# Kernel optimization log

Measured on AMD Instinct MI355X. Metric: run time of the kernel, lower is better.

The kernel has to match this reference:

```python
import math
import jax, jax.numpy as jnp
import numpy as np

# ---- module hyperparameters (from init_kwargs) ----
BIG_K = 13
SMALL_K = 3
C_OUT = 128
GROUP_IN = 4
NK = math.ceil(BIG_K / SMALL_K)          # 5 small kernels cover the big one
C_IN = NK * C_OUT                        # 640
PADDING = SMALL_K - 1                    # shift() padding
EXTRA_PAD = PADDING - SMALL_K // 2       # 1
MID = BIG_K // 2
REAL_PAD = [MID - i * SMALL_K - PADDING for i in range(NK)]  # [4,1,-2,-5,-8]
MARGIN = BIG_K                           # zero-pad margin covering all shifts

B = 32
HOUT = 56
WOUT = 56
HIN = HOUT + 2 * EXTRA_PAD
WIN = WOUT + 2 * EXTRA_PAD


def _build_indices():
    # Faithful numpy replication of shuffle_idx_2_gen_pads (torch.manual_seed(123) analog).
    rng = np.random.RandomState(123)
    idx_offset = np.array(REAL_PAD * C_OUT, dtype=np.int32)  # (C_IN,)

    def group_pads():
        pads = []
        for _ in range(GROUP_IN):
            idx = np.concatenate([rng.permutation(NK) + i * NK for i in range(C_OUT)])
            pads.append(idx_offset[np.argsort(idx, kind='stable')])
        return np.stack(pads)  # (GROUP_IN, C_IN)

    pad_h = group_pads()
    pad_v = group_pads()
    pad_hv = np.concatenate([pad_h, pad_v], axis=0).T.astype(np.int32)  # (C_IN, 2*GROUP_IN)
    idx_identit = np.stack(
        [rng.randint(0, NK, C_OUT) + np.arange(C_OUT) * NK for _ in range(GROUP_IN)]
    ).T.astype(np.int32)  # (C_OUT, GROUP_IN)
    return pad_hv, idx_identit


def setup_inputs() -> dict:
    key = jax.random.key(0)
    pad_hv, idx_identit = _build_indices()
    x = jax.random.normal(key, (B, C_IN, HIN, WIN), dtype=jnp.float32)
    return {
        'x': x,
        'pad_hv': jnp.asarray(pad_hv),
        'idx_identit': jnp.asarray(idx_identit),
        'hout': HOUT,
        'wout': WOUT,
    }


def reference(x, pad_hv, idx_identit, hout, wout):
    # x: (B, C_IN, hout+2*EXTRA_PAD, wout+2*EXTRA_PAD)
    Bx = x.shape[0]
    M = MARGIN

    # ---- horizontal-shift branch: per-channel shift along W, accumulate over groups ----
    xp_w = jnp.pad(x, ((0, 0), (0, 0), (0, 0), (M, M)))          # zero pad width
    xh = xp_w[:, :, EXTRA_PAD:EXTRA_PAD + hout, :]
    w_base = jnp.arange(wout, dtype=jnp.int32) + EXTRA_PAD + M   # (wout,)
    out_h = jnp.zeros((Bx, C_IN, hout, wout), x.dtype)
    for g in range(GROUP_IN):
        idx = w_base[None, :] + pad_hv[:, g][:, None]            # (C_IN, wout)
        out_h = out_h + jnp.take_along_axis(xh, idx[None, :, None, :], axis=3)

    # ---- vertical-shift branch: per-channel shift along H ----
    xp_h = jnp.pad(x, ((0, 0), (0, 0), (M, M), (0, 0)))
    xv = xp_h[:, :, :, EXTRA_PAD:EXTRA_PAD + wout]               # (B,C_IN,HIN+2M,wout)
    h_base = jnp.arange(hout, dtype=jnp.int32) + EXTRA_PAD + M
    out_v = jnp.zeros((Bx, C_IN, hout, wout), x.dtype)
    for g in range(GROUP_IN):
        idx = h_base[None, :] + pad_hv[:, GROUP_IN + g][:, None]  # (C_IN, hout)
        out_v = out_v + jnp.take_along_axis(xv, idx[None, :, :, None], axis=2)

    # scatter-add input channels j into output channel idx_out[j] = j // NK
    out_h = out_h.reshape(Bx, C_OUT, NK, hout, wout).sum(axis=2)
    out_v = out_v.reshape(Bx, C_OUT, NK, hout, wout).sum(axis=2)

    # ---- identity branch: center crop + channel gather, summed over groups ----
    xc = x[:, :, EXTRA_PAD:EXTRA_PAD + hout, EXTRA_PAD:EXTRA_PAD + wout]
    out_id = xc[:, idx_identit, :, :].sum(axis=2)                # (B,C_OUT,hout,wout)

    return out_h, out_v, out_id
```

## Files before the change

kernel.cpp:

```cpp
#include <hip/hip_runtime.h>

#define BATCH   32
#define C_OUT_N 128
#define NK      5
#define C_IN_N  (NK * C_OUT_N)
#define HIN     58
#define WIN     58
#define HOUT    56
#define WOUT    56
#define NPIX    (HOUT * WOUT)
#define NTILE   (HOUT * (WOUT / 8))
#define OUT_PLANE ((size_t)BATCH * C_OUT_N * NPIX)

#define NTHREADS   512
#define LDS_STRIDE 70
#define LDS_ROWS   (NK * HIN)
#define LDS_HALVES (LDS_ROWS * LDS_STRIDE)
#define CH_STRIDE  (HIN * LDS_STRIDE)
#define NV4        (NK * HIN * WIN / 4)

typedef _Float16 h2 __attribute__((ext_vector_type(2)));

static __device__ __forceinline__ unsigned int h2u(h2 v) {
    unsigned int r; __builtin_memcpy(&r, &v, 4); return r;
}
static __device__ __forceinline__ h2 uh2(unsigned int u) {
    h2 r; __builtin_memcpy(&r, &u, 4); return r;
}
static __device__ __forceinline__ h2 algn(h2 lo, h2 hi) {
    return uh2(__builtin_amdgcn_alignbit(h2u(hi), h2u(lo), 16));
}
static __device__ __forceinline__ h2 pkrtz(float a, float b) {
    auto t = __builtin_amdgcn_cvt_pkrtz(a, b);
    h2 r; __builtin_memcpy(&r, &t, 4); return r;
}
static __device__ __forceinline__ float uni(float v) {
    return __uint_as_float(__builtin_amdgcn_readfirstlane(__float_as_uint(v)));
}

__global__ __launch_bounds__(NTHREADS, 8) void addshift_hoist_kernel(
    const float* __restrict__ x,
    const int*   __restrict__ pad_hv,
    const int*   __restrict__ idx_id,
    float*       __restrict__ out)
{
    extern __shared__ _Float16 lds[];

    const int bc  = blockIdx.x;
    const int b   = bc / C_OUT_N;
    const int co  = bc - b * C_OUT_N;
    const int tid = threadIdx.x;

    for (int i = tid; i < LDS_ROWS * 12; i += NTHREADS) {
        int j = i / 12;
        int m = i - j * 12;
        int c = (m < 7) ? m : (58 + m);
        lds[j * LDS_STRIDE + c] = (_Float16)0.f;
    }

    const float* xbase = x + (size_t)(b * C_IN_N + co * NK) * (HIN * WIN);
    for (int i = tid; i < NV4; i += NTHREADS) {
        int g = 4 * i;
        float4 v = *(const float4*)(xbase + g);
        int r = g / 58;
        int c = g - r * 58;
        _Float16* dst = &lds[r * LDS_STRIDE + 7 + c];
        if (c <= 54) {
            dst[0] = (_Float16)v.x;
            *(h2*)(dst + 1) = pkrtz(v.y, v.z);
            dst[3] = (_Float16)v.w;
        } else {
            dst[0] = (_Float16)v.x;
            dst[1] = (_Float16)v.y;
            _Float16* d2 = &lds[(r + 1) * LDS_STRIDE + 7];
            d2[0] = (_Float16)v.z;
            d2[1] = (_Float16)v.w;
        }
    }

    float mhf[NK][5], mvf[NK][5], cntf[NK];
    #pragma unroll
    for (int k = 0; k < NK; ++k) {
        #pragma unroll
        for (int t = 0; t < 5; ++t) { mhf[k][t] = 0.f; mvf[k][t] = 0.f; }
        cntf[k] = 0.f;
        #pragma unroll
        for (int g = 0; g < 4; ++g) {
            int sh_v = pad_hv[(co * NK + k) * 8 + g];
            int th   = (4 - sh_v) / 3;
            int sv_v = pad_hv[(co * NK + k) * 8 + 4 + g];
            int tv   = (4 - sv_v) / 3;
            #pragma unroll
            for (int t = 0; t < 5; ++t) {
                mhf[k][t] += (th == t) ? 1.f : 0.f;
                mvf[k][t] += (tv == t) ? 1.f : 0.f;
            }
        }
    }
    #pragma unroll
    for (int g = 0; g < 4; ++g) {
        int c = idx_id[co * 4 + g] - co * NK;
        #pragma unroll
        for (int k = 0; k < NK; ++k) cntf[k] += (c == k) ? 1.f : 0.f;
    }
    #pragma unroll
    for (int k = 0; k < NK; ++k) {
        cntf[k] = uni(cntf[k]);
        #pragma unroll
        for (int t = 0; t < 5; ++t) { mhf[k][t] = uni(mhf[k][t]); mvf[k][t] = uni(mvf[k][t]); }
    }

    __syncthreads();

    const int q = tid;
    if (q < NTILE) {
        const int h  = q / 7;
        const int w0 = 8 * (q - h * 7);

        int  voff[5];
        bool okv[5];
        #pragma unroll
        for (int t = 0; t < 5; ++t) {
            int rr = h + 5 - 3 * t;
            okv[t] = (unsigned)rr < 58u;
            int rc = rr < 0 ? 0 : (rr > 57 ? 57 : rr);
            voff[t] = rc * LDS_STRIDE + w0 + 8;
        }
        const int rowbase = (h + 1) * LDS_STRIDE + w0;

        h2 sh[4], sv[4], si[4];
        #pragma unroll
        for (int m = 0; m < 4; ++m) {
            sh[m] = h2{(_Float16)0.f, (_Float16)0.f};
            sv[m] = sh[m]; si[m] = sh[m];
        }

        #pragma unroll
        for (int k = 0; k < NK; ++k) {
            const _Float16* chp  = lds + k * CH_STRIDE;
            const _Float16* rowp = chp + rowbase;

            h2 H[10];
            #pragma unroll
            for (int m = 0; m < 10; ++m) H[m] = *(const h2*)(rowp + 2 * m);

            h2 V[5][4];
            #pragma unroll
            for (int t = 0; t < 5; ++t) {
                const _Float16* vp = chp + voff[t];
                #pragma unroll
                for (int m = 0; m < 4; ++m) V[t][m] = *(const h2*)(vp + 2 * m);
            }

            #pragma unroll
            for (int t = 0; t < 5; ++t) {
                float wg = mhf[k][t];
                if (wg != 0.f) {
                    _Float16 wh = (_Float16)wg;
                    h2 w2 = h2{wh, wh};
                    int j = 12 - 3 * t;
                    if ((j & 1) == 0) {
                        int m0 = j >> 1;
                        #pragma unroll
                        for (int m = 0; m < 4; ++m) sh[m] += w2 * H[m0 + m];
                    } else {
                        int m0 = (j - 1) >> 1;
                        #pragma unroll
                        for (int m = 0; m < 4; ++m)
                            sh[m] += w2 * algn(H[m0 + m], H[m0 + m + 1]);
                    }
                }
            }

            float ck = cntf[k];
            if (ck != 0.f) {
                _Float16 ch16 = (_Float16)ck;
                h2 c2 = h2{ch16, ch16};
                #pragma unroll
                for (int m = 0; m < 4; ++m) si[m] += c2 * H[4 + m];
            }

            #pragma unroll
            for (int t = 0; t < 5; ++t) {
                float wv = mvf[k][t];
                if (wv != 0.f) {
                    float wm = okv[t] ? wv : 0.f;
                    _Float16 wh = (_Float16)wm;
                    h2 w2 = h2{wh, wh};
                    #pragma unroll
                    for (int m = 0; m < 4; ++m) sv[m] += w2 * V[t][m];
                }
            }
        }

        size_t o = (size_t)bc * NPIX + h * WOUT + w0;
        *(float4*)(out + o) =
            make_float4((float)sh[0].x, (float)sh[0].y, (float)sh[1].x, (float)sh[1].y);
        *(float4*)(out + o + 4) =
            make_float4((float)sh[2].x, (float)sh[2].y, (float)sh[3].x, (float)sh[3].y);
        *(float4*)(out + OUT_PLANE + o) =
            make_float4((float)sv[0].x, (float)sv[0].y, (float)sv[1].x, (float)sv[1].y);
        *(float4*)(out + OUT_PLANE + o + 4) =
            make_float4((float)sv[2].x, (float)sv[2].y, (float)sv[3].x, (float)sv[3].y);
        *(float4*)(out + 2 * OUT_PLANE + o) =
            make_float4((float)si[0].x, (float)si[0].y, (float)si[1].x, (float)si[1].y);
        *(float4*)(out + 2 * OUT_PLANE + o + 4) =
            make_float4((float)si[2].x, (float)si[2].y, (float)si[3].x, (float)si[3].y);
    }
}

extern "C" void kernel_launch(void* const* d_in, const int* in_sizes, int n_in,
                              void* d_out, int out_size, void* d_ws, size_t ws_size,
                              hipStream_t stream) {
    const float* x      = (const float*)d_in[0];
    const int*   pad_hv = (const int*)d_in[1];
    const int*   idx_id = (const int*)d_in[2];
    float*       out    = (float*)d_out;

    addshift_hoist_kernel<<<dim3(BATCH * C_OUT_N), dim3(NTHREADS),
                            LDS_HALVES * 2, stream>>>(x, pad_hv, idx_id, out);
}
```

Baseline: 106.9 us.

## Double-buffer per-channel LDS staging with register prefetch of next channel

Replaces staging all five input channels in LDS at once with a two-slot ring buffer. Each thread prefetches the next channel into registers while the current one is processed. This cuts LDS footprint to raise occupancy and overlaps global loads with compute, at the cost of extra block-wide barriers per channel. Vertical-branch values are now read from LDS on demand instead of preloaded.

```diff
diff --git a/kernel.cpp b/kernel.cpp
--- a/kernel.cpp
+++ b/kernel.cpp
@@ -14,10 +14,9 @@
 
 #define NTHREADS   512
 #define LDS_STRIDE 70
-#define LDS_ROWS   (NK * HIN)
-#define LDS_HALVES (LDS_ROWS * LDS_STRIDE)
-#define CH_STRIDE  (HIN * LDS_STRIDE)
-#define NV4        (NK * HIN * WIN / 4)
+#define CH_HALVES  (HIN * LDS_STRIDE)
+#define LDS_HALVES (2 * CH_HALVES)
+#define NV4C       (HIN * WIN / 4)
 
 typedef _Float16 h2 __attribute__((ext_vector_type(2)));
 
@@ -38,7 +37,7 @@
     return __uint_as_float(__builtin_amdgcn_readfirstlane(__float_as_uint(v)));
 }
 
-__global__ __launch_bounds__(NTHREADS, 8) void addshift_hoist_kernel(
+__global__ __launch_bounds__(NTHREADS, 8) void addshift_pipe_kernel(
     const float* __restrict__ x,
     const int*   __restrict__ pad_hv,
     const int*   __restrict__ idx_id,
@@ -51,20 +50,19 @@
     const int co  = bc - b * C_OUT_N;
     const int tid = threadIdx.x;
 
-    for (int i = tid; i < LDS_ROWS * 12; i += NTHREADS) {
-        int j = i / 12;
-        int m = i - j * 12;
-        int c = (m < 7) ? m : (58 + m);
-        lds[j * LDS_STRIDE + c] = (_Float16)0.f;
-    }
-
     const float* xbase = x + (size_t)(b * C_IN_N + co * NK) * (HIN * WIN);
-    for (int i = tid; i < NV4; i += NTHREADS) {
-        int g = 4 * i;
-        float4 v = *(const float4*)(xbase + g);
+
+    auto issue_ch = [&](int k, float4& v1, float4& v2) {
+        const float* src = xbase + k * (HIN * WIN);
+        v1 = *(const float4*)(src + 4 * tid);
+        if (tid < NV4C - NTHREADS)
+            v2 = *(const float4*)(src + 4 * (tid + NTHREADS));
+    };
+    auto write_one = [&](int bsel, float4 v, int i4) {
+        int g = 4 * i4;
         int r = g / 58;
-        int c = g - r * 58;
-        _Float16* dst = &lds[r * LDS_STRIDE + 7 + c];
+        int c = g - 58 * r;
+        _Float16* dst = &lds[bsel * CH_HALVES + r * LDS_STRIDE + 7 + c];
         if (c <= 54) {
             dst[0] = (_Float16)v.x;
             *(h2*)(dst + 1) = pkrtz(v.y, v.z);
@@ -72,11 +70,27 @@
         } else {
             dst[0] = (_Float16)v.x;
             dst[1] = (_Float16)v.y;
-            _Float16* d2 = &lds[(r + 1) * LDS_STRIDE + 7];
+            _Float16* d2 = &lds[bsel * CH_HALVES + (r + 1) * LDS_STRIDE + 7];
             d2[0] = (_Float16)v.z;
             d2[1] = (_Float16)v.w;
         }
-    }
+    };
+    auto write_ch = [&](int bsel, float4 v1, float4 v2) {
+        write_one(bsel, v1, tid);
+        if (tid < NV4C - NTHREADS) write_one(bsel, v2, tid + NTHREADS);
+    };
+
+    for (int i = tid; i < 2 * HIN * 12; i += NTHREADS) {
+        int bsel = i / (HIN * 12);
+        int m2   = i - bsel * (HIN * 12);
+        int row  = m2 / 12;
+        int m    = m2 - row * 12;
+        int c    = (m < 7) ? m : (58 + m);
+        lds[bsel * CH_HALVES + row * LDS_STRIDE + c] = (_Float16)0.f;
+    }
+
+    float4 s1, s2;
+    issue_ch(0, s1, s2);
 
     float mhf[NK][5], mvf[NK][5], cntf[NK];
     #pragma unroll
@@ -110,47 +124,42 @@
         for (int t = 0; t < 5; ++t) { mhf[k][t] = uni(mhf[k][t]); mvf[k][t] = uni(mvf[k][t]); }
     }
 
+    write_ch(0, s1, s2);
+    issue_ch(1, s1, s2);
     __syncthreads();
 
-    const int q = tid;
-    if (q < NTILE) {
-        const int h  = q / 7;
-        const int w0 = 8 * (q - h * 7);
-
-        int  voff[5];
-        bool okv[5];
-        #pragma unroll
-        for (int t = 0; t < 5; ++t) {
-            int rr = h + 5 - 3 * t;
-            okv[t] = (unsigned)rr < 58u;
-            int rc = rr < 0 ? 0 : (rr > 57 ? 57 : rr);
-            voff[t] = rc * LDS_STRIDE + w0 + 8;
-        }
-        const int rowbase = (h + 1) * LDS_STRIDE + w0;
-
-        h2 sh[4], sv[4], si[4];
-        #pragma unroll
-        for (int m = 0; m < 4; ++m) {
-            sh[m] = h2{(_Float16)0.f, (_Float16)0.f};
-            sv[m] = sh[m]; si[m] = sh[m];
-        }
-
-        #pragma unroll
-        for (int k = 0; k < NK; ++k) {
-            const _Float16* chp  = lds + k * CH_STRIDE;
+    const int q  = tid;
+    const int h  = q / 7;
+    const int w0 = 8 * (q - h * 7);
+    int  voff[5];
+    bool okv[5];
+    #pragma unroll
+    for (int t = 0; t < 5; ++t) {
+        int rr = h + 5 - 3 * t;
+        okv[t] = (unsigned)rr < 58u;
+        int rc = rr < 0 ? 0 : (rr > 57 ? 57 : rr);
+        voff[t] = rc * LDS_STRIDE + w0 + 8;
+    }
+    const int rowbase = (h + 1) * LDS_STRIDE + w0;
+
+    h2 sh[4], sv[4], si[4];
+    #pragma unroll
+    for (int m = 0; m < 4; ++m) {
+        sh[m] = h2{(_Float16)0.f, (_Float16)0.f};
+        sv[m] = sh[m]; si[m] = sh[m];
+    }
+
+    #pragma unroll
+    for (int k = 0; k < NK; ++k) {
+        const int cb = (k & 1) * CH_HALVES;
+
+        if (q < NTILE) {
+            const _Float16* chp  = lds + cb;
             const _Float16* rowp = chp + rowbase;
 
             h2 H[10];
             #pragma unroll
             for (int m = 0; m < 10; ++m) H[m] = *(const h2*)(rowp + 2 * m);
-
-            h2 V[5][4];
-            #pragma unroll
-            for (int t = 0; t < 5; ++t) {
-                const _Float16* vp = chp + voff[t];
-                #pragma unroll
-                for (int m = 0; m < 4; ++m) V[t][m] = *(const h2*)(vp + 2 * m);
-            }
 
             #pragma unroll
             for (int t = 0; t < 5; ++t) {
@@ -174,8 +183,8 @@
 
             float ck = cntf[k];
             if (ck != 0.f) {
-                _Float16 ch16 = (_Float16)ck;
-                h2 c2 = h2{ch16, ch16};
+                _Float16 c16 = (_Float16)ck;
+                h2 c2 = h2{c16, c16};
                 #pragma unroll
                 for (int m = 0; m < 4; ++m) si[m] += c2 * H[4 + m];
             }
@@ -187,12 +196,23 @@
                     float wm = okv[t] ? wv : 0.f;
                     _Float16 wh = (_Float16)wm;
                     h2 w2 = h2{wh, wh};
+                    const _Float16* vp = chp + voff[t];
                     #pragma unroll
-                    for (int m = 0; m < 4; ++m) sv[m] += w2 * V[t][m];
+                    for (int m = 0; m < 4; ++m)
+                        sv[m] += w2 * *(const h2*)(vp + 2 * m);
                 }
             }
         }
 
+        if (k < NK - 1) {
+            __syncthreads();
+            write_ch((k + 1) & 1, s1, s2);
+            if (k < NK - 2) issue_ch(k + 2, s1, s2);
+            __syncthreads();
+        }
+    }
+
+    if (q < NTILE) {
         size_t o = (size_t)bc * NPIX + h * WOUT + w0;
         *(float4*)(out + o) =
             make_float4((float)sh[0].x, (float)sh[0].y, (float)sh[1].x, (float)sh[1].y);
@@ -217,6 +237,6 @@
     const int*   idx_id = (const int*)d_in[2];
     float*       out    = (float*)d_out;
 
-    addshift_hoist_kernel<<<dim3(BATCH * C_OUT_N), dim3(NTHREADS),
-                            LDS_HALVES * 2, stream>>>(x, pad_hv, idx_id, out);
-}
+    addshift_pipe_kernel<<<dim3(BATCH * C_OUT_N), dim3(NTHREADS),
+                           LDS_HALVES * 2, stream>>>(x, pad_hv, idx_id, out);
+}
```

New measurement: 128.6 us. 1.2x slower.

## Make kernel persistent over batches and prefetch next input tile into registers

Applied to the files above, without the earlier changes.

Launches 512 blocks instead of 4096. Each block handles one output channel for eight batch entries, with the pad/identity weight setup done once per block. While the current batch's LDS tile is being computed, the next batch's input is prefetched into registers (eight float4 per thread plus a tail) so the global load overlaps compute. Vertical taps are now loaded on demand instead of all preloaded. This costs register pressure (launch bounds relaxed to 4) and leaves fewer blocks to hide latency and balance load across CUs.

```diff
diff --git a/kernel.cpp b/kernel.cpp
--- a/kernel.cpp
+++ b/kernel.cpp
@@ -18,6 +18,9 @@
 #define LDS_HALVES (LDS_ROWS * LDS_STRIDE)
 #define CH_STRIDE  (HIN * LDS_STRIDE)
 #define NV4        (NK * HIN * WIN / 4)
+#define NFULL      8
+#define NTAIL      (NV4 - NFULL * NTHREADS)
+#define NCHUNK     8
 
 typedef _Float16 h2 __attribute__((ext_vector_type(2)));
 
@@ -38,7 +41,7 @@
     return __uint_as_float(__builtin_amdgcn_readfirstlane(__float_as_uint(v)));
 }
 
-__global__ __launch_bounds__(NTHREADS, 8) void addshift_hoist_kernel(
+__global__ __launch_bounds__(NTHREADS, 4) void addshift_pers_kernel(
     const float* __restrict__ x,
     const int*   __restrict__ pad_hv,
     const int*   __restrict__ idx_id,
@@ -46,9 +49,9 @@
 {
     extern __shared__ _Float16 lds[];
 
-    const int bc  = blockIdx.x;
-    const int b   = bc / C_OUT_N;
-    const int co  = bc - b * C_OUT_N;
+    const int bid = blockIdx.x;
+    const int co  = bid & 127;
+    const int b0  = bid >> 7;
     const int tid = threadIdx.x;
 
     for (int i = tid; i < LDS_ROWS * 12; i += NTHREADS) {
@@ -58,10 +61,8 @@
         lds[j * LDS_STRIDE + c] = (_Float16)0.f;
     }
 
-    const float* xbase = x + (size_t)(b * C_IN_N + co * NK) * (HIN * WIN);
-    for (int i = tid; i < NV4; i += NTHREADS) {
-        int g = 4 * i;
-        float4 v = *(const float4*)(xbase + g);
+    auto write_one = [&](float4 v, int i4) {
+        int g = 4 * i4;
         int r = g / 58;
         int c = g - r * 58;
         _Float16* dst = &lds[r * LDS_STRIDE + 7 + c];
@@ -76,7 +77,7 @@
             d2[0] = (_Float16)v.z;
             d2[1] = (_Float16)v.w;
         }
-    }
+    };
 
     float mhf[NK][5], mvf[NK][5], cntf[NK];
     #pragma unroll
@@ -110,102 +111,124 @@
         for (int t = 0; t < 5; ++t) { mhf[k][t] = uni(mhf[k][t]); mvf[k][t] = uni(mvf[k][t]); }
     }
 
-    __syncthreads();
-
-    const int q = tid;
-    if (q < NTILE) {
-        const int h  = q / 7;
-        const int w0 = 8 * (q - h * 7);
-
-        int  voff[5];
-        bool okv[5];
-        #pragma unroll
-        for (int t = 0; t < 5; ++t) {
-            int rr = h + 5 - 3 * t;
-            okv[t] = (unsigned)rr < 58u;
-            int rc = rr < 0 ? 0 : (rr > 57 ? 57 : rr);
-            voff[t] = rc * LDS_STRIDE + w0 + 8;
-        }
-        const int rowbase = (h + 1) * LDS_STRIDE + w0;
-
-        h2 sh[4], sv[4], si[4];
-        #pragma unroll
-        for (int m = 0; m < 4; ++m) {
-            sh[m] = h2{(_Float16)0.f, (_Float16)0.f};
-            sv[m] = sh[m]; si[m] = sh[m];
-        }
-
-        #pragma unroll
-        for (int k = 0; k < NK; ++k) {
-            const _Float16* chp  = lds + k * CH_STRIDE;
-            const _Float16* rowp = chp + rowbase;
-
-            h2 H[10];
-            #pragma unroll
-            for (int m = 0; m < 10; ++m) H[m] = *(const h2*)(rowp + 2 * m);
-
-            h2 V[5][4];
-            #pragma unroll
-            for (int t = 0; t < 5; ++t) {
-                const _Float16* vp = chp + voff[t];
+    const int h  = tid / 7;
+    const int w0 = 8 * (tid - h * 7);
+    int  voff[5];
+    bool okv[5];
+    #pragma unroll
+    for (int t = 0; t < 5; ++t) {
+        int rr = h + 5 - 3 * t;
+        okv[t] = (unsigned)rr < 58u;
+        int rc = rr < 0 ? 0 : (rr > 57 ? 57 : rr);
+        voff[t] = rc * LDS_STRIDE + w0 + 8;
+    }
+    const int rowbase = (h + 1) * LDS_STRIDE + w0;
+
+    float4 sA[NFULL], sB;
+    {
+        const float* src = x + (size_t)(b0 * C_IN_N + co * NK) * (HIN * WIN);
+        #pragma unroll
+        for (int r = 0; r < NFULL; ++r)
+            sA[r] = *(const float4*)(src + 4 * (tid + NTHREADS * r));
+        if (tid < NTAIL)
+            sB = *(const float4*)(src + 4 * (NFULL * NTHREADS + tid));
+    }
+
+    for (int j = 0; j < NCHUNK; ++j) {
+        const int b = b0 + 4 * j;
+
+        __syncthreads();
+
+        #pragma unroll
+        for (int r = 0; r < NFULL; ++r) write_one(sA[r], tid + NTHREADS * r);
+        if (tid < NTAIL) write_one(sB, NFULL * NTHREADS + tid);
+
+        if (j + 1 < NCHUNK) {
+            const float* src = x + (size_t)((b + 4) * C_IN_N + co * NK) * (HIN * WIN);
+            #pragma unroll
+            for (int r = 0; r < NFULL; ++r)
+                sA[r] = *(const float4*)(src + 4 * (tid + NTHREADS * r));
+            if (tid < NTAIL)
+                sB = *(const float4*)(src + 4 * (NFULL * NTHREADS + tid));
+        }
+
+        __syncthreads();
+
+        if (tid < NTILE) {
+            h2 sh[4], sv[4], si[4];
+            #pragma unroll
+            for (int m = 0; m < 4; ++m) {
+                sh[m] = h2{(_Float16)0.f, (_Float16)0.f};
+                sv[m] = sh[m]; si[m] = sh[m];
+            }
+
+            #pragma unroll
+            for (int k = 0; k < NK; ++k) {
+                const _Float16* chp  = lds + k * CH_STRIDE;
+                const _Float16* rowp = chp + rowbase;
+
+                h2 H[10];
                 #pragma unroll
-                for (int m = 0; m < 4; ++m) V[t][m] = *(const h2*)(vp + 2 * m);
-            }
-
-            #pragma unroll
-            for (int t = 0; t < 5; ++t) {
-                float wg = mhf[k][t];
-                if (wg != 0.f) {
-                    _Float16 wh = (_Float16)wg;
-                    h2 w2 = h2{wh, wh};
-                    int j = 12 - 3 * t;
-                    if ((j & 1) == 0) {
-                        int m0 = j >> 1;
-                        #pragma unroll
-                        for (int m = 0; m < 4; ++m) sh[m] += w2 * H[m0 + m];
-                    } else {
-                        int m0 = (j - 1) >> 1;
+                for (int m = 0; m < 10; ++m) H[m] = *(const h2*)(rowp + 2 * m);
+
+                #pragma unroll
+                for (int t = 0; t < 5; ++t) {
+                    float wg = mhf[k][t];
+                    if (wg != 0.f) {
+                        _Float16 wh = (_Float16)wg;
+                        h2 w2 = h2{wh, wh};
+                        int j2 = 12 - 3 * t;
+                        if ((j2 & 1) == 0) {
+                            int m0 = j2 >> 1;
+                            #pragma unroll
+                            for (int m = 0; m < 4; ++m) sh[m] += w2 * H[m0 + m];
+                        } else {
+                            int m0 = (j2 - 1) >> 1;
+                            #pragma unroll
+                            for (int m = 0; m < 4; ++m)
+                                sh[m] += w2 * algn(H[m0 + m], H[m0 + m + 1]);
+                        }
+                    }
+                }
+
+                float ck = cntf[k];
+                if (ck != 0.f) {
+                    _Float16 c16 = (_Float16)ck;
+                    h2 c2 = h2{c16, c16};
+                    #pragma unroll
+                    for (int m = 0; m < 4; ++m) si[m] += c2 * H[4 + m];
+                }
+
+                #pragma unroll
+                for (int t = 0; t < 5; ++t) {
+                    float wv = mvf[k][t];
+                    if (wv != 0.f) {
+                        float wm = okv[t] ? wv : 0.f;
+                        _Float16 wh = (_Float16)wm;
+                        h2 w2 = h2{wh, wh};
+                        const _Float16* vp = chp + voff[t];
                         #pragma unroll
                         for (int m = 0; m < 4; ++m)
-                            sh[m] += w2 * algn(H[m0 + m], H[m0 + m + 1]);
+                            sv[m] += w2 * *(const h2*)(vp + 2 * m);
                     }
                 }
             }
 
-            float ck = cntf[k];
-            if (ck != 0.f) {
-                _Float16 ch16 = (_Float16)ck;
-                h2 c2 = h2{ch16, ch16};
-                #pragma unroll
-                for (int m = 0; m < 4; ++m) si[m] += c2 * H[4 + m];
-            }
-
-            #pragma unroll
-            for (int t = 0; t < 5; ++t) {
-                float wv = mvf[k][t];
-                if (wv != 0.f) {
-                    float wm = okv[t] ? wv : 0.f;
-                    _Float16 wh = (_Float16)wm;
-                    h2 w2 = h2{wh, wh};
-                    #pragma unroll
-                    for (int m = 0; m < 4; ++m) sv[m] += w2 * V[t][m];
-                }
-            }
-        }
-
-        size_t o = (size_t)bc * NPIX + h * WOUT + w0;
-        *(float4*)(out + o) =
-            make_float4((float)sh[0].x, (float)sh[0].y, (float)sh[1].x, (float)sh[1].y);
-        *(float4*)(out + o + 4) =
-            make_float4((float)sh[2].x, (float)sh[2].y, (float)sh[3].x, (float)sh[3].y);
-        *(float4*)(out + OUT_PLANE + o) =
-            make_float4((float)sv[0].x, (float)sv[0].y, (float)sv[1].x, (float)sv[1].y);
-        *(float4*)(out + OUT_PLANE + o + 4) =
-            make_float4((float)sv[2].x, (float)sv[2].y, (float)sv[3].x, (float)sv[3].y);
-        *(float4*)(out + 2 * OUT_PLANE + o) =
-            make_float4((float)si[0].x, (float)si[0].y, (float)si[1].x, (float)si[1].y);
-        *(float4*)(out + 2 * OUT_PLANE + o + 4) =
-            make_float4((float)si[2].x, (float)si[2].y, (float)si[3].x, (float)si[3].y);
+            const int bc = b * C_OUT_N + co;
+            size_t o = (size_t)bc * NPIX + h * WOUT + w0;
+            *(float4*)(out + o) =
+                make_float4((float)sh[0].x, (float)sh[0].y, (float)sh[1].x, (float)sh[1].y);
+            *(float4*)(out + o + 4) =
+                make_float4((float)sh[2].x, (float)sh[2].y, (float)sh[3].x, (float)sh[3].y);
+            *(float4*)(out + OUT_PLANE + o) =
+                make_float4((float)sv[0].x, (float)sv[0].y, (float)sv[1].x, (float)sv[1].y);
+            *(float4*)(out + OUT_PLANE + o + 4) =
+                make_float4((float)sv[2].x, (float)sv[2].y, (float)sv[3].x, (float)sv[3].y);
+            *(float4*)(out + 2 * OUT_PLANE + o) =
+                make_float4((float)si[0].x, (float)si[0].y, (float)si[1].x, (float)si[1].y);
+            *(float4*)(out + 2 * OUT_PLANE + o + 4) =
+                make_float4((float)si[2].x, (float)si[2].y, (float)si[3].x, (float)si[3].y);
+        }
     }
 }
 
@@ -217,6 +240,6 @@
     const int*   idx_id = (const int*)d_in[2];
     float*       out    = (float*)d_out;
 
-    addshift_hoist_kernel<<<dim3(BATCH * C_OUT_N), dim3(NTHREADS),
-                            LDS_HALVES * 2, stream>>>(x, pad_hv, idx_id, out);
-}
+    addshift_pers_kernel<<<dim3(512), dim3(NTHREADS), LDS_HALVES * 2, stream>>>(
+        x, pad_hv, idx_id, out);
+}
```

New measurement: 131.7 us. +23.3%, slower.
